# Kernel optimization log

Hardware: AMD Instinct MI355X
Metric: run time of the kernel (lower is better)

The kernel has to match this reference:

```python
import jax, jax.numpy as jnp
import numpy as np

B, L = 16, 2048
D_MODEL, D_INNER, D_STATE, DT_RANK, D_CONV = 128, 256, 16, 8, 4
N_LAYERS, N_CLASSES = 4, 5
EPS = 1e-5


def setup_inputs() -> dict:
    key = jax.random.key(0)
    ks = jax.random.split(key, 12)
    rn = lambda k, shape, s=0.02: jax.random.normal(k, shape, jnp.float32) * s
    A_log = jnp.log(jnp.arange(1, D_STATE + 1, dtype=jnp.float32))  # S4D-real init
    return dict(
        x=jax.random.normal(ks[0], (B, L, 12), jnp.float32),
        enc_w=rn(ks[1], (D_MODEL, 12), 0.1),
        enc_b=jnp.zeros((D_MODEL,), jnp.float32),
        norm_w=jnp.ones((N_LAYERS, D_MODEL), jnp.float32),
        in_proj_w=rn(ks[2], (N_LAYERS, 2 * D_INNER, D_MODEL)),
        conv_w=rn(ks[3], (N_LAYERS, D_INNER, D_CONV), 0.1),
        conv_b=jnp.zeros((N_LAYERS, D_INNER), jnp.float32),
        x_proj_w=rn(ks[4], (N_LAYERS, DT_RANK + 2 * D_STATE, D_INNER)),
        dt_proj_w=rn(ks[5], (N_LAYERS, D_INNER, DT_RANK), 0.1),
        dt_proj_b=rn(ks[6], (N_LAYERS, D_INNER), 0.1),
        A_log=jnp.broadcast_to(A_log, (N_LAYERS, D_INNER, D_STATE)) + 0.0,
        Dp=jnp.ones((N_LAYERS, D_INNER), jnp.float32),
        out_proj_w=rn(ks[7], (N_LAYERS, D_MODEL, D_INNER)),
        norm_f_w=jnp.ones((D_MODEL,), jnp.float32),
        cls_w=rn(ks[8], (N_CLASSES, D_MODEL), 0.05),
        cls_b=jnp.zeros((N_CLASSES,), jnp.float32),
    )


def rmsnorm(x, w):
    return x * jax.lax.rsqrt(jnp.mean(x * x, axis=-1, keepdims=True) + EPS) * w


def causal_depthwise_conv(x, w, b):
    # x: [b, l, di]; w: [di, k]; causal (left) padding, groups=di
    xc = x.transpose(0, 2, 1)  # [b, di, l]
    y = jax.lax.conv_general_dilated(
        xc, w[:, None, :], window_strides=(1,), padding=[(D_CONV - 1, 0)],
        dimension_numbers=("NCH", "OIH", "NCH"), feature_group_count=D_INNER)
    return (y + b[None, :, None]).transpose(0, 2, 1)


def selective_scan(u, delta, A, Bm, Cm, Dv):
    # u, delta: [b,l,di]; A: [di,n]; Bm, Cm: [b,l,n]; Dv: [di]
    dA = jnp.exp(jnp.einsum("bld,dn->bldn", delta, A))          # [b,l,di,n]
    dBu = jnp.einsum("bld,bln,bld->bldn", delta, Bm, u)          # [b,l,di,n]

    def step(h, inp):
        dA_t, dBu_t, C_t = inp
        h = dA_t * h + dBu_t                                     # [b,di,n]
        y = jnp.einsum("bdn,bn->bd", h, C_t)
        return h, y

    h0 = jnp.zeros((u.shape[0], u.shape[2], A.shape[1]), u.dtype)
    xs = (dA.transpose(1, 0, 2, 3), dBu.transpose(1, 0, 2, 3), Cm.transpose(1, 0, 2))
    _, ys = jax.lax.scan(step, h0, xs)
    return ys.transpose(1, 0, 2) + u * Dv


def mamba_block(x, in_w, cw, cb, xp_w, dt_w, dt_b, A_log_i, D_i, out_w):
    xz = jnp.einsum("bld,ed->ble", x, in_w)                      # [b,l,2*di]
    xm, z = xz[..., :D_INNER], xz[..., D_INNER:]
    xm = jax.nn.silu(causal_depthwise_conv(xm, cw, cb))
    x_dbl = jnp.einsum("bld,ed->ble", xm, xp_w)                  # [b,l,dt_rank+2n]
    dt = x_dbl[..., :DT_RANK]
    Bm = x_dbl[..., DT_RANK:DT_RANK + D_STATE]
    Cm = x_dbl[..., DT_RANK + D_STATE:]
    delta = jax.nn.softplus(jnp.einsum("blr,dr->bld", dt, dt_w) + dt_b)
    A = -jnp.exp(A_log_i)
    y = selective_scan(xm, delta, A, Bm, Cm, D_i)
    y = y * jax.nn.silu(z)
    return jnp.einsum("bld,ed->ble", y, out_w)


def reference(x, enc_w, enc_b, norm_w, in_proj_w, conv_w, conv_b, x_proj_w,
              dt_proj_w, dt_proj_b, A_log, Dp, out_proj_w, norm_f_w, cls_w, cls_b):
    h = jnp.einsum("blc,dc->bld", x, enc_w) + enc_b               # conv1d k=1 encoder
    for i in range(N_LAYERS):
        h = mamba_block(rmsnorm(h, norm_w[i]), in_proj_w[i], conv_w[i], conv_b[i],
                        x_proj_w[i], dt_proj_w[i], dt_proj_b[i], A_log[i], Dp[i],
                        out_proj_w[i]) + h
    h = rmsnorm(h, norm_f_w)
    pooled = jnp.mean(h, axis=1)                                  # AdaptiveAvgPool1d(1)
    return pooled @ cls_w.T + cls_b                               # [B, n_classes]
```

## Files before the change

### kernel.cpp

```cpp
#include <hip/hip_runtime.h>
#include <hip/hip_bf16.h>
#include <cstddef>

#define BB 16
#define LL 2048
#define DM 128
#define DI 256
#define DS 16
#define MP (BB*LL)
#define NSEG 64
#define SEGLEN (LL/NSEG)
#define YSTR 264
#define XSTR 40
#define SXS 48

typedef __attribute__((ext_vector_type(8))) short bf16x8;
typedef __attribute__((ext_vector_type(4))) short bf16x4s;
typedef __attribute__((ext_vector_type(8))) unsigned int ux8;
typedef __attribute__((ext_vector_type(4))) float f32x4;
typedef __hip_bfloat16 bf16;
typedef unsigned int uint;

__device__ inline void bf16split(float x, bf16& h, bf16& l) {
  h = __float2bfloat16(x);
  l = __float2bfloat16(x - __bfloat162float(h));
}
__device__ inline float bf2f(bf16 v) { return __bfloat162float(v); }
__device__ inline void split_bits2(float x, short& hs, short& ls) {
  bf16 hb = __float2bfloat16(x);
  bf16 lb = __float2bfloat16(x - __bfloat162float(hb));
  hs = *(short*)&hb;
  ls = *(short*)&lb;
}
__device__ inline short bfbits(float x) {
  bf16 b = __float2bfloat16(x);
  return *(short*)&b;
}
__device__ inline float sigm(float x) {
  return __builtin_amdgcn_rcpf(1.f + __expf(-x));
}
__device__ inline uint pk2(short h, short l) {
  return (uint)(unsigned short)h | ((uint)(unsigned short)l << 16);
}
__device__ inline uint pack_hl(float x) {
  short hs, ls; split_bits2(x, hs, ls);
  return pk2(hs, ls);
}
__device__ inline float unpack_hl(uint w) {
  return __uint_as_float(w << 16) + __uint_as_float(w & 0xffff0000u);
}

__device__ inline float softplus_f(float a) {
  float r = __logf(1.f + __expf(a));
  return a > 15.f ? a : r;
}

__device__ inline void make_powers(float r, float* rp) {
  rp[0] = r;
#pragma unroll
  for (int n = 1; n < 16; n++) {
    int a = (n + 1) >> 1, b = (n + 1) - a;
    rp[n] = rp[a - 1] * rp[b - 1];
  }
}

__device__ inline bool a_is_integer(const float* A_log, int d) {
  bool ok = true;
#pragma unroll
  for (int n = 0; n < DS; n++) {
    float Ad = -__expf(A_log[d * DS + n]);
    ok = ok && (fabsf(Ad + (float)(n + 1)) < 1e-3f);
  }
  return ok;
}

template<bool FAST>
__device__ inline void scan1_lds(int s, int b, int d,
    const float* sx, const short* ubh, const short* ubl,
    const float* __restrict__ dtw, const float* __restrict__ dtb,
    const float* __restrict__ A_log,
    float* __restrict__ sega, float* __restrict__ segh) {
  float wdt[8];
#pragma unroll
  for (int j = 0; j < 8; j++) wdt[j] = dtw[d * 8 + j];
  float bdt = dtb[d];
  float h[DS];
#pragma unroll
  for (int n = 0; n < DS; n++) h[n] = 0.f;
  float R = 1.f;
  float ap[DS];
  if (!FAST) {
#pragma unroll
    for (int n = 0; n < DS; n++) ap[n] = 1.f;
  }
#pragma unroll 4
  for (int t = 0; t < SEGLEN; t++) {
    const float* xr = sx + t * SXS;
    float dt = bdt;
#pragma unroll
    for (int j = 0; j < 8; j++) dt += xr[j] * wdt[j];
    float dl = softplus_f(dt);
    float u = unpack_hl(pk2(ubh[t * 264 + d], ubl[t * 264 + d]));
    float du = dl * u;
    if (FAST) {
      float rp[DS];
      make_powers(__expf(-dl), rp);
      R *= rp[0];
#pragma unroll
      for (int n = 0; n < DS; n++) h[n] = fmaf(rp[n], h[n], du * xr[8 + n]);
    } else {
#pragma unroll
      for (int n = 0; n < DS; n++) {
        float dA = __expf(dl * (-__expf(A_log[d * DS + n])));
        h[n] = fmaf(dA, h[n], du * xr[8 + n]);
        ap[n] *= dA;
      }
    }
  }
  if (FAST) make_powers(R, ap);
  size_t o = ((size_t)s * 4096 + b * 256 + d) * DS;
#pragma unroll
  for (int j = 0; j < 4; j++) {
    *(float4*)(sega + o + 4 * j) = make_float4(ap[4*j], ap[4*j+1], ap[4*j+2], ap[4*j+3]);
    *(float4*)(segh + o + 4 * j) = make_float4(h[4*j], h[4*j+1], h[4*j+2], h[4*j+3]);
  }
}

__global__ __launch_bounds__(256, 2) void gemm_inproj_conv(
    const bf16* __restrict__ Ah, const bf16* __restrict__ Al,
    const bf16* __restrict__ Wh, const bf16* __restrict__ Wl,
    const bf16* __restrict__ Xh, const bf16* __restrict__ Xl,
    const float* __restrict__ cw, const float* __restrict__ cb,
    const float* __restrict__ dtw, const float* __restrict__ dtb,
    const float* __restrict__ A_log,
    uint* __restrict__ zs_pk, uint* __restrict__ u_pk,
    float* __restrict__ C,
    float* __restrict__ sega, float* __restrict__ segh) {
  __shared__ uint  xmb[35 * 260];
  __shared__ short ubh[32 * 264];
  __shared__ short ubl[32 * 264];
  __shared__ float scw[DI * 4 + DI];
  int tid = threadIdx.x;
  {
    float4 w4 = *(const float4*)(cw + tid * 4);
    *(float4*)(scw + tid * 4) = w4;
    scw[DI * 4 + tid] = cb[tid];
  }
  int wave = tid >> 6, lane = tid & 63;
  int r16 = lane & 15, quad = lane >> 4;
  int m0 = blockIdx.x * 32;

  size_t arow[3];
#pragma unroll
  for (int rt = 0; rt < 3; rt++) {
    int rg = m0 - 16 + rt * 16 + r16;
    if (rg < 0) rg = 0;
    arow[rt] = (size_t)rg * DM + quad * 8;
  }
  size_t browx[4], browz[4];
#pragma unroll
  for (int ct = 0; ct < 4; ct++) {
    browx[ct] = (size_t)(wave * 64 + ct * 16 + r16) * DM + quad * 8;
    browz[ct] = (size_t)(256 + wave * 64 + ct * 16 + r16) * DM + quad * 8;
  }
  f32x4 accx[3][4] = {};
  f32x4 accz[2][4] = {};
#pragma unroll
  for (int kk = 0; kk < 4; kk++) {
    int ko = kk * 32;
    bf16x8 ah[3], al[3], bxh[4], bxl[4], bzh[4], bzl[4];
#pragma unroll
    for (int rt = 0; rt < 3; rt++) {
      ah[rt] = *(const bf16x8*)(Ah + arow[rt] + ko);
      al[rt] = *(const bf16x8*)(Al + arow[rt] + ko);
    }
#pragma unroll
    for (int ct = 0; ct < 4; ct++) {
      bxh[ct] = *(const bf16x8*)(Wh + browx[ct] + ko);
      bxl[ct] = *(const bf16x8*)(Wl + browx[ct] + ko);
      bzh[ct] = *(const bf16x8*)(Wh + browz[ct] + ko);
      bzl[ct] = *(const bf16x8*)(Wl + browz[ct] + ko);
    }
#pragma unroll
    for (int rt = 0; rt < 3; rt++)
#pragma unroll
      for (int ct = 0; ct < 4; ct++) {
        accx[rt][ct] = __builtin_amdgcn_mfma_f32_16x16x32_bf16(ah[rt], bxh[ct], accx[rt][ct], 0, 0, 0);
        accx[rt][ct] = __builtin_amdgcn_mfma_f32_16x16x32_bf16(ah[rt], bxl[ct], accx[rt][ct], 0, 0, 0);
        accx[rt][ct] = __builtin_amdgcn_mfma_f32_16x16x32_bf16(al[rt], bxh[ct], accx[rt][ct], 0, 0, 0);
      }
#pragma unroll
    for (int rz = 0; rz < 2; rz++)
#pragma unroll
      for (int ct = 0; ct < 4; ct++) {
        accz[rz][ct] = __builtin_amdgcn_mfma_f32_16x16x32_bf16(ah[rz + 1], bzh[ct], accz[rz][ct], 0, 0, 0);
        accz[rz][ct] = __builtin_amdgcn_mfma_f32_16x16x32_bf16(ah[rz + 1], bzl[ct], accz[rz][ct], 0, 0, 0);
        accz[rz][ct] = __builtin_amdgcn_mfma_f32_16x16x32_bf16(al[rz + 1], bzh[ct], accz[rz][ct], 0, 0, 0);
      }
  }
#pragma unroll
  for (int rz = 0; rz < 2; rz++)
#pragma unroll
    for (int ct = 0; ct < 4; ct++)
#pragma unroll
      for (int r = 0; r < 4; r++) {
        int row = m0 + rz * 16 + quad * 4 + r;
        int col = wave * 64 + ct * 16 + r16;
        float v = accz[rz][ct][r];
        v *= sigm(v);
        zs_pk[(size_t)row * DI + col] = pack_hl(v);
      }
#pragma unroll
  for (int rt = 0; rt < 3; rt++)
#pragma unroll
    for (int ct = 0; ct < 4; ct++)
#pragma unroll
      for (int r = 0; r < 4; r++) {
        int lidx = rt * 16 + quad * 4 + r - 13;
        if (lidx >= 0)
          xmb[lidx * 260 + wave * 64 + ct * 16 + r16] = pack_hl(accx[rt][ct][r]);
      }
  __syncthreads();

  {
    int d = tid;
    float w0 = scw[d * 4], w1 = scw[d * 4 + 1], w2 = scw[d * 4 + 2], w3 = scw[d * 4 + 3];
    float bias = scw[DI * 4 + d];
    float xa = unpack_hl(xmb[0 * 260 + d]);
    float xb = unpack_hl(xmb[1 * 260 + d]);
    float xc = unpack_hl(xmb[2 * 260 + d]);
    int lbase = m0 & (LL - 1);
#pragma unroll 4
    for (int t = 0; t < 32; t++) {
      float xd = unpack_hl(xmb[(t + 3) * 260 + d]);
      int l = lbase + t;
      float x0 = xa * ((l >= 3) ? 1.f : 0.f);
      float x1 = xb * ((l >= 2) ? 1.f : 0.f);
      float x2 = xc * ((l >= 1) ? 1.f : 0.f);
      float c0 = bias + w0 * x0 + w1 * x1 + w2 * x2 + w3 * xd;
      float u = c0 * sigm(c0);
      short hs, ls; split_bits2(u, hs, ls);
      u_pk[(size_t)(m0 + t) * DI + d] = pk2(hs, ls);
      ubh[t * 264 + d] = hs;
      ubl[t * 264 + d] = ls;
      xa = xb; xb = xc; xc = xd;
    }
  }
  __syncthreads();

  float* sx = (float*)xmb;
  {
    int rt0 = (wave == 3) ? 1 : 0;
    int ct0 = (wave == 0) ? 0 : (wave == 1) ? 1 : (wave == 2) ? 2 : 0;
#pragma unroll 1
    for (int tt = 0; tt < 2; tt++) {
      int rt, ct;
      if (tt == 0) { rt = rt0; ct = ct0; }
      else { if (wave >= 2) break; rt = 1; ct = wave + 1; }
      f32x4 a2 = {};
#pragma unroll
      for (int kk = 0; kk < 8; kk++) {
        int k0 = quad * 8 + kk * 32;
        bf16x8 ahh = *(const bf16x8*)(ubh + (rt * 16 + r16) * 264 + k0);
        bf16x8 alo = *(const bf16x8*)(ubl + (rt * 16 + r16) * 264 + k0);
        size_t br = (size_t)(ct * 16 + r16) * DI + quad * 8 + kk * 32;
        bf16x8 bhh = *(const bf16x8*)(Xh + br);
        bf16x8 blo = *(const bf16x8*)(Xl + br);
        a2 = __builtin_amdgcn_mfma_f32_16x16x32_bf16(ahh, bhh, a2, 0, 0, 0);
        a2 = __builtin_amdgcn_mfma_f32_16x16x32_bf16(ahh, blo, a2, 0, 0, 0);
        a2 = __builtin_amdgcn_mfma_f32_16x16x32_bf16(alo, bhh, a2, 0, 0, 0);
      }
#pragma unroll
      for (int r = 0; r < 4; r++) {
        int row = rt * 16 + quad * 4 + r;
        int col = ct * 16 + r16;
        C[(size_t)(m0 + row) * 64 + col] = a2[r];
        sx[row * SXS + col] = a2[r];
      }
    }
  }
  __syncthreads();

  {
    int b = blockIdx.x >> 6, s = blockIdx.x & 63, d = tid;
    if (a_is_integer(A_log, d))
      scan1_lds<true>(s, b, d, sx, ubh, ubl, dtw, dtb, A_log, sega, segh);
    else
      scan1_lds<false>(s, b, d, sx, ubh, ubl, dtw, dtb, A_log, sega, segh);
  }
}

__global__ __launch_bounds__(256) void encoder_kernel(const float* __restrict__ x,
    const float* __restrict__ ew, const float* __restrict__ eb,
    float* __restrict__ h) {
  int idx = blockIdx.x * 256 + threadIdx.x;
  int d = idx & 127, m = idx >> 7;
  float acc = eb[d];
#pragma unroll
  for (int c = 0; c < 12; c++) acc += x[m * 12 + c] * ew[d * 12 + c];
  h[idx] = acc;
}

__global__ void split_w(const float* __restrict__ src, bf16* __restrict__ hi,
                        bf16* __restrict__ lo, int n) {
  int i = blockIdx.x * 256 + threadIdx.x;
  if (i < n) bf16split(src[i], hi[i], lo[i]);
}

__global__ void split_w_pad(const float* __restrict__ src, bf16* __restrict__ hi,
                            bf16* __restrict__ lo) {
  int i = blockIdx.x * 256 + threadIdx.x;
  int l = i >> 14, rem = i & 16383, r = rem >> 8, k = rem & 255;
  float v = (r < 40) ? src[l * 10240 + r * 256 + k] : 0.f;
  bf16split(v, hi[i], lo[i]);
}

__global__ __launch_bounds__(256) void rmsnorm_kernel(const float* __restrict__ x,
    const float* __restrict__ w, bf16* __restrict__ oh, bf16* __restrict__ ol) {
  int lane = threadIdx.x & 63;
  int pos = blockIdx.x * 4 + (threadIdx.x >> 6);
  const float* row = x + (size_t)pos * DM;
  float v0 = row[lane], v1 = row[lane + 64];
  float ss = v0 * v0 + v1 * v1;
#pragma unroll
  for (int off = 1; off < 64; off <<= 1) ss += __shfl_xor(ss, off);
  float sc = rsqrtf(ss * (1.f / DM) + 1e-5f);
  float a = v0 * sc * w[lane], b = v1 * sc * w[lane + 64];
  size_t o = (size_t)pos * DM;
  bf16split(a, oh[o + lane], ol[o + lane]);
  bf16split(b, oh[o + lane + 64], ol[o + lane + 64]);
}

__device__ inline void load_sx(float* sx, const float* xdbl, size_t rbase, int tid) {
#pragma unroll
  for (int j = 0; j < 2; j++) {
    int idx = j * 256 + tid;
    if (idx < 320) {
      int row = idx / 10, c = idx % 10;
      *(float4*)(sx + row * XSTR + c * 4) = *(const float4*)(xdbl + rbase + row * 64 + c * 4);
    }
  }
}

__global__ __launch_bounds__(256) void scan_combine(float* __restrict__ sega,
    const float* __restrict__ segh) {
  int g = blockIdx.x * 256 + threadIdx.x;
  size_t off = (size_t)(g >> 2) * 16 + (g & 3) * 4;
  float4 h0 = make_float4(0.f, 0.f, 0.f, 0.f);
  for (int s = 0; s < NSEG; s++) {
    size_t q = (size_t)s * 65536 + off;
    float4 a = *(float4*)(sega + q);
    float4 hh = *(float4*)(segh + q);
    *(float4*)(sega + q) = h0;
    h0.x = a.x * h0.x + hh.x;
    h0.y = a.y * h0.y + hh.y;
    h0.z = a.z * h0.z + hh.z;
    h0.w = a.w * h0.w + hh.w;
  }
}

template<bool FAST>
__device__ inline void scan2_to_lds(int s, int b, int d, const float* sx,
    const uint* __restrict__ u_pk, const uint* __restrict__ zs_pk,
    const float* __restrict__ dtw, const float* __restrict__ dtb,
    const float* __restrict__ A_log, const float* __restrict__ Dp,
    const float* __restrict__ sega, short* __restrict__ ybuf) {
  float wdt[8];
#pragma unroll
  for (int j = 0; j < 8; j++) wdt[j] = dtw[d * 8 + j];
  float bdt = dtb[d];
  float h[DS];
  size_t o = ((size_t)s * 4096 + b * 256 + d) * DS;
#pragma unroll
  for (int n = 0; n < DS; n++) h[n] = sega[o + n];
  float Dd = Dp[d];
  size_t base = (size_t)b * LL + (size_t)s * SEGLEN;
  const uint* up = u_pk + base * DI + d;
  const uint* zp = zs_pk + base * DI + d;
  uint ub = *up, zb = *zp;
#pragma unroll 4
  for (int t = 0; t < SEGLEN; t++) {
    up += DI; zp += DI;
    uint ub_next = *up;
    uint zb_next = *zp;
    const float* xr = sx + t * XSTR;
    float dt = bdt;
#pragma unroll
    for (int j = 0; j < 8; j++) dt += xr[j] * wdt[j];
    float dl = softplus_f(dt);
    float u = unpack_hl(ub);
    float du = dl * u;
    float acc = 0.f;
    if (FAST) {
      float rp[DS];
      make_powers(__expf(-dl), rp);
#pragma unroll
      for (int n = 0; n < DS; n++) {
        h[n] = fmaf(rp[n], h[n], du * xr[8 + n]);
        acc = fmaf(h[n], xr[24 + n], acc);
      }
    } else {
#pragma unroll
      for (int n = 0; n < DS; n++) {
        float dA = __expf(dl * (-__expf(A_log[d * DS + n])));
        h[n] = fmaf(dA, h[n], du * xr[8 + n]);
        acc = fmaf(h[n], xr[24 + n], acc);
      }
    }
    float zs = unpack_hl(zb);
    float yv = (acc + u * Dd) * zs;
    ybuf[t * YSTR + d] = bfbits(yv);
    ub = ub_next; zb = zb_next;
  }
}

__global__ __launch_bounds__(256, 6) void scan2_outproj(
    const uint* __restrict__ u_pk, const uint* __restrict__ zs_pk,
    const float* __restrict__ xdbl, const float* __restrict__ dtw,
    const float* __restrict__ dtb, const float* __restrict__ A_log,
    const float* __restrict__ Dp, const float* __restrict__ sega,
    const bf16* __restrict__ Wh, const bf16* __restrict__ Wl,
    float* __restrict__ hbuf, const float* __restrict__ nw,
    float* __restrict__ of, bf16* __restrict__ oh, bf16* __restrict__ ol) {
  __shared__ float sx[SEGLEN * XSTR];
  __shared__ short ybuf[32 * YSTR];
  int s = blockIdx.x, b = blockIdx.y;
  int tid = threadIdx.x, d = tid;
  size_t rbase = ((size_t)b * LL + (size_t)s * SEGLEN) * 64;
  load_sx(sx, xdbl, rbase, tid);
  __syncthreads();
  if (a_is_integer(A_log, d))
    scan2_to_lds<true>(s, b, d, sx, u_pk, zs_pk, dtw, dtb, A_log, Dp, sega, ybuf);
  else
    scan2_to_lds<false>(s, b, d, sx, u_pk, zs_pk, dtw, dtb, A_log, Dp, sega, ybuf);
  __syncthreads();
  int wave = tid >> 6, lane = tid & 63;
  int r16 = lane & 15, quad = lane >> 4;
  int n0 = wave * 32;
  size_t brow[2];
#pragma unroll
  for (int j = 0; j < 2; j++)
    brow[j] = (size_t)(n0 + j * 16 + r16) * DI + quad * 8;
  f32x4 acc[2][2] = {};
#pragma unroll
  for (int kk = 0; kk < 8; kk++) {
    int k0 = quad * 8 + kk * 32;
    bf16x8 ah[2], bh[2], bl[2];
#pragma unroll
    for (int i = 0; i < 2; i++)
      ah[i] = *(const bf16x8*)(ybuf + (i * 16 + r16) * YSTR + k0);
#pragma unroll
    for (int j = 0; j < 2; j++) {
      bh[j] = *(const bf16x8*)(Wh + brow[j] + kk * 32);
      bl[j] = *(const bf16x8*)(Wl + brow[j] + kk * 32);
    }
#pragma unroll
    for (int i = 0; i < 2; i++)
#pragma unroll
      for (int j = 0; j < 2; j++) {
        acc[i][j] = __builtin_amdgcn_mfma_f32_16x16x32_bf16(ah[i], bh[j], acc[i][j], 0, 0, 0);
        acc[i][j] = __builtin_amdgcn_mfma_f32_16x16x32_bf16(ah[i], bl[j], acc[i][j], 0, 0, 0);
      }
  }
  __syncthreads();
  float* tile = (float*)ybuf;
#pragma unroll
  for (int i = 0; i < 2; i++)
#pragma unroll
    for (int j = 0; j < 2; j++)
#pragma unroll
      for (int r = 0; r < 4; r++) {
        int rl = i * 16 + quad * 4 + r;
        int col = n0 + j * 16 + r16;
        tile[rl * 132 + col] = acc[i][j][r];
      }
  __syncthreads();
  size_t mbase = (size_t)b * LL + (size_t)s * SEGLEN;
#pragma unroll
  for (int it = 0; it < 4; it++) {
    int idx = it * 256 + tid;
    int row = idx >> 5, c4 = idx & 31;
    size_t g = (mbase + row) * DM + c4 * 4;
    float4 hv = *(float4*)(hbuf + g);
    const float* tp = tile + row * 132 + c4 * 4;
    float4 v = make_float4(tp[0] + hv.x, tp[1] + hv.y, tp[2] + hv.z, tp[3] + hv.w);
    *(float4*)(hbuf + g) = v;
    float ss = v.x * v.x + v.y * v.y + v.z * v.z + v.w * v.w;
    ss += __shfl_xor(ss, 1);
    ss += __shfl_xor(ss, 2);
    ss += __shfl_xor(ss, 4);
    ss += __shfl_xor(ss, 8);
    ss += __shfl_xor(ss, 16);
    float sc = rsqrtf(ss * (1.f / DM) + 1e-5f);
    float4 w4 = *(const float4*)(nw + c4 * 4);
    float n0v = v.x * sc * w4.x, n1v = v.y * sc * w4.y;
    float n2v = v.z * sc * w4.z, n3v = v.w * sc * w4.w;
    if (of) *(float4*)(of + g) = make_float4(n0v, n1v, n2v, n3v);
    short h0s, l0s, h1s, l1s, h2s, l2s, h3s, l3s;
    split_bits2(n0v, h0s, l0s); split_bits2(n1v, h1s, l1s);
    split_bits2(n2v, h2s, l2s); split_bits2(n3v, h3s, l3s);
    bf16x4s hb, lb;
    hb[0] = h0s; hb[1] = h1s; hb[2] = h2s; hb[3] = h3s;
    lb[0] = l0s; lb[1] = l1s; lb[2] = l2s; lb[3] = l3s;
    *(bf16x4s*)(oh + g) = hb;
    *(bf16x4s*)(ol + g) = lb;
  }
}

__global__ __launch_bounds__(256) void pool_partial(const float* __restrict__ fn,
    float* __restrict__ partial) {
  __shared__ float red[256];
  int b = blockIdx.x, c = blockIdx.y;
  int tid = threadIdx.x;
  int d = tid & 127, rp_ = tid >> 7;
  float s = 0.f;
  size_t base = (size_t)b * LL + c * 256;
  for (int i = 0; i < 128; i++) {
    int row = i * 2 + rp_;
    s += fn[(base + row) * DM + d];
  }
  red[tid] = s;
  __syncthreads();
  if (tid < 128) partial[((size_t)b * 8 + c) * 128 + tid] = red[tid] + red[tid + 128];
}

__global__ void pool_reduce(const float* __restrict__ partial,
    float* __restrict__ pooled) {
  int idx = blockIdx.x * 256 + threadIdx.x;
  int b = idx >> 7, d = idx & 127;
  float s = 0.f;
#pragma unroll
  for (int c = 0; c < 8; c++) s += partial[((size_t)b * 8 + c) * 128 + d];
  pooled[idx] = s * (1.f / LL);
}

__global__ void cls_kernel(const float* __restrict__ pooled,
    const float* __restrict__ cw, const float* __restrict__ cb,
    float* __restrict__ out) {
  int t = threadIdx.x;
  if (t < 80) {
    int b = t / 5, c = t % 5;
    float acc = cb[c];
    for (int d = 0; d < DM; d++) acc += pooled[b * DM + d] * cw[c * DM + d];
    out[t] = acc;
  }
}

extern "C" void kernel_launch(void* const* d_in, const int* in_sizes, int n_in,
                              void* d_out, int out_size, void* d_ws, size_t ws_size,
                              hipStream_t stream) {
  const float* x         = (const float*)d_in[0];
  const float* enc_w     = (const float*)d_in[1];
  const float* enc_b     = (const float*)d_in[2];
  const float* norm_w    = (const float*)d_in[3];
  const float* in_proj_w = (const float*)d_in[4];
  const float* conv_w    = (const float*)d_in[5];
  const float* conv_b    = (const float*)d_in[6];
  const float* x_proj_w  = (const float*)d_in[7];
  const float* dt_proj_w = (const float*)d_in[8];
  const float* dt_proj_b = (const float*)d_in[9];
  const float* A_log     = (const float*)d_in[10];
  const float* Dp        = (const float*)d_in[11];
  const float* out_proj_w= (const float*)d_in[12];
  const float* norm_f_w  = (const float*)d_in[13];
  const float* cls_w     = (const float*)d_in[14];
  const float* cls_b     = (const float*)d_in[15];
  float* out = (float*)d_out;

  float* ws = (float*)d_ws;
  float* h       = ws;
  float* xdbl    = ws + 4194304;
  float* sega    = ws + 6291456;
  float* segh    = ws + 10485760;
  uint*  zs_pk   = (uint*)(ws + 14680064);
  uint*  u_pk    = (uint*)(ws + 23068672);
  uint*  xm_pk   = (uint*)(ws + 31457280);
  float* partial = ws + 39845888;
  float* pooled  = ws + 39862272;
  bf16* u0     = (bf16*)(ws + 39864320);
  bf16* xn_hi  = u0;
  bf16* xn_lo  = u0 + 4194304;
  bf16* wip_hi = u0 + 8388608;
  bf16* wip_lo = wip_hi + 262144;
  bf16* wxp_hi = wip_lo + 262144;
  bf16* wxp_lo = wxp_hi + 65536;
  bf16* wop_hi = wxp_lo + 65536;
  bf16* wop_lo = wop_hi + 131072;
  float* fnorm = (float*)xm_pk;

  split_w<<<1024, 256, 0, stream>>>(in_proj_w, wip_hi, wip_lo, 262144);
  split_w_pad<<<256, 256, 0, stream>>>(x_proj_w, wxp_hi, wxp_lo);
  split_w<<<512, 256, 0, stream>>>(out_proj_w, wop_hi, wop_lo, 131072);

  encoder_kernel<<<MP * DM / 256, 256, 0, stream>>>(x, enc_w, enc_b, h);
  rmsnorm_kernel<<<MP / 4, 256, 0, stream>>>(h, norm_w, xn_hi, xn_lo);

  for (int i = 0; i < 4; i++) {
    gemm_inproj_conv<<<MP / 32, 256, 0, stream>>>(xn_hi, xn_lo,
        wip_hi + i * 65536, wip_lo + i * 65536,
        wxp_hi + i * 16384, wxp_lo + i * 16384,
        conv_w + i * DI * 4, conv_b + i * DI,
        dt_proj_w + i * 2048, dt_proj_b + i * DI, A_log + i * DI * DS,
        zs_pk, u_pk, xdbl, sega, segh);
    scan_combine<<<64, 256, 0, stream>>>(sega, segh);
    scan2_outproj<<<dim3(NSEG, BB), 256, 0, stream>>>(u_pk, zs_pk, xdbl,
        dt_proj_w + i * 2048, dt_proj_b + i * DI, A_log + i * DI * DS,
        Dp + i * DI, sega, wop_hi + i * 32768, wop_lo + i * 32768, h,
        (i < 3) ? norm_w + (i + 1) * DM : norm_f_w,
        (i < 3) ? nullptr : fnorm, xn_hi, xn_lo);
  }

  pool_partial<<<dim3(BB, 8), 256, 0, stream>>>(fnorm, partial);
  pool_reduce<<<8, 256, 0, stream>>>(partial, pooled);
  cls_kernel<<<1, 128, 0, stream>>>(pooled, cls_w, cls_b, out);
}
```

Baseline: 661.8 us.

## Move z-branch in_proj GEMM into scan kernel and keep gate in LDS

The z half of the in_proj GEMM and its SiLU gate move out of the in_proj/conv kernel and into the scan/out_proj kernel. The gate is computed per 16-row half directly into shared memory, so the packed zs buffer no longer has to be written to and read back from global memory each layer. The cost is more shared memory and registers in the scan kernel, which drops its occupancy hint from 6 to 4 blocks. Extra barriers and the z GEMM itself now sit serially between the two scan halves.

```diff
diff --git a/kernel.cpp b/kernel.cpp
--- a/kernel.cpp
+++ b/kernel.cpp
@@ -133,7 +133,7 @@
     const float* __restrict__ cw, const float* __restrict__ cb,
     const float* __restrict__ dtw, const float* __restrict__ dtb,
     const float* __restrict__ A_log,
-    uint* __restrict__ zs_pk, uint* __restrict__ u_pk,
+    uint* __restrict__ u_pk,
     float* __restrict__ C,
     float* __restrict__ sega, float* __restrict__ segh) {
   __shared__ uint  xmb[35 * 260];
@@ -157,18 +157,15 @@
     if (rg < 0) rg = 0;
     arow[rt] = (size_t)rg * DM + quad * 8;
   }
-  size_t browx[4], browz[4];
-#pragma unroll
-  for (int ct = 0; ct < 4; ct++) {
+  size_t browx[4];
+#pragma unroll
+  for (int ct = 0; ct < 4; ct++)
     browx[ct] = (size_t)(wave * 64 + ct * 16 + r16) * DM + quad * 8;
-    browz[ct] = (size_t)(256 + wave * 64 + ct * 16 + r16) * DM + quad * 8;
-  }
   f32x4 accx[3][4] = {};
-  f32x4 accz[2][4] = {};
 #pragma unroll
   for (int kk = 0; kk < 4; kk++) {
     int ko = kk * 32;
-    bf16x8 ah[3], al[3], bxh[4], bxl[4], bzh[4], bzl[4];
+    bf16x8 ah[3], al[3], bxh[4], bxl[4];
 #pragma unroll
     for (int rt = 0; rt < 3; rt++) {
       ah[rt] = *(const bf16x8*)(Ah + arow[rt] + ko);
@@ -178,8 +175,6 @@
     for (int ct = 0; ct < 4; ct++) {
       bxh[ct] = *(const bf16x8*)(Wh + browx[ct] + ko);
       bxl[ct] = *(const bf16x8*)(Wl + browx[ct] + ko);
-      bzh[ct] = *(const bf16x8*)(Wh + browz[ct] + ko);
-      bzl[ct] = *(const bf16x8*)(Wl + browz[ct] + ko);
     }
 #pragma unroll
     for (int rt = 0; rt < 3; rt++)
@@ -189,27 +184,7 @@
         accx[rt][ct] = __builtin_amdgcn_mfma_f32_16x16x32_bf16(ah[rt], bxl[ct], accx[rt][ct], 0, 0, 0);
         accx[rt][ct] = __builtin_amdgcn_mfma_f32_16x16x32_bf16(al[rt], bxh[ct], accx[rt][ct], 0, 0, 0);
       }
-#pragma unroll
-    for (int rz = 0; rz < 2; rz++)
-#pragma unroll
-      for (int ct = 0; ct < 4; ct++) {
-        accz[rz][ct] = __builtin_amdgcn_mfma_f32_16x16x32_bf16(ah[rz + 1], bzh[ct], accz[rz][ct], 0, 0, 0);
-        accz[rz][ct] = __builtin_amdgcn_mfma_f32_16x16x32_bf16(ah[rz + 1], bzl[ct], accz[rz][ct], 0, 0, 0);
-        accz[rz][ct] = __builtin_amdgcn_mfma_f32_16x16x32_bf16(al[rz + 1], bzh[ct], accz[rz][ct], 0, 0, 0);
-      }
-  }
-#pragma unroll
-  for (int rz = 0; rz < 2; rz++)
-#pragma unroll
-    for (int ct = 0; ct < 4; ct++)
-#pragma unroll
-      for (int r = 0; r < 4; r++) {
-        int row = m0 + rz * 16 + quad * 4 + r;
-        int col = wave * 64 + ct * 16 + r16;
-        float v = accz[rz][ct][r];
-        v *= sigm(v);
-        zs_pk[(size_t)row * DI + col] = pack_hl(v);
-      }
+  }
 #pragma unroll
   for (int rt = 0; rt < 3; rt++)
 #pragma unroll
@@ -359,30 +334,52 @@
   }
 }
 
+__device__ inline void zgemm_half(int hh, size_t mbase, int wave, int r16, int quad,
+    const bf16* xnh, const bf16* xnl,
+    const bf16* __restrict__ Wih, const bf16* __restrict__ Wil,
+    uint* zbuf) {
+  size_t ar = (mbase + hh * 16 + r16) * DM + quad * 8;
+  size_t br[4];
+#pragma unroll
+  for (int ct = 0; ct < 4; ct++)
+    br[ct] = (size_t)(256 + wave * 64 + ct * 16 + r16) * DM + quad * 8;
+  f32x4 acc[4] = {};
+#pragma unroll
+  for (int kk = 0; kk < 4; kk++) {
+    int ko = kk * 32;
+    bf16x8 ah = *(const bf16x8*)(xnh + ar + ko);
+    bf16x8 al = *(const bf16x8*)(xnl + ar + ko);
+    bf16x8 bh[4], bl[4];
+#pragma unroll
+    for (int ct = 0; ct < 4; ct++) {
+      bh[ct] = *(const bf16x8*)(Wih + br[ct] + ko);
+      bl[ct] = *(const bf16x8*)(Wil + br[ct] + ko);
+    }
+#pragma unroll
+    for (int ct = 0; ct < 4; ct++) {
+      acc[ct] = __builtin_amdgcn_mfma_f32_16x16x32_bf16(ah, bh[ct], acc[ct], 0, 0, 0);
+      acc[ct] = __builtin_amdgcn_mfma_f32_16x16x32_bf16(ah, bl[ct], acc[ct], 0, 0, 0);
+      acc[ct] = __builtin_amdgcn_mfma_f32_16x16x32_bf16(al, bh[ct], acc[ct], 0, 0, 0);
+    }
+  }
+#pragma unroll
+  for (int ct = 0; ct < 4; ct++)
+#pragma unroll
+    for (int r = 0; r < 4; r++) {
+      float v = acc[ct][r];
+      v *= sigm(v);
+      zbuf[(quad * 4 + r) * 260 + wave * 64 + ct * 16 + r16] = pack_hl(v);
+    }
+}
+
 template<bool FAST>
-__device__ inline void scan2_to_lds(int s, int b, int d, const float* sx,
-    const uint* __restrict__ u_pk, const uint* __restrict__ zs_pk,
-    const float* __restrict__ dtw, const float* __restrict__ dtb,
-    const float* __restrict__ A_log, const float* __restrict__ Dp,
-    const float* __restrict__ sega, short* __restrict__ ybuf) {
-  float wdt[8];
-#pragma unroll
-  for (int j = 0; j < 8; j++) wdt[j] = dtw[d * 8 + j];
-  float bdt = dtb[d];
-  float h[DS];
-  size_t o = ((size_t)s * 4096 + b * 256 + d) * DS;
-#pragma unroll
-  for (int n = 0; n < DS; n++) h[n] = sega[o + n];
-  float Dd = Dp[d];
-  size_t base = (size_t)b * LL + (size_t)s * SEGLEN;
-  const uint* up = u_pk + base * DI + d;
-  const uint* zp = zs_pk + base * DI + d;
-  uint ub = *up, zb = *zp;
+__device__ inline void scan2_half(int t0, int d, const float* sx, const uint* zbuf,
+    const uint*& up, uint& ub, const float* wdt, float bdt,
+    const float* __restrict__ A_log, float Dd, float* h, short* ybuf) {
 #pragma unroll 4
-  for (int t = 0; t < SEGLEN; t++) {
-    up += DI; zp += DI;
+  for (int t = t0; t < t0 + 16; t++) {
+    up += DI;
     uint ub_next = *up;
-    uint zb_next = *zp;
     const float* xr = sx + t * XSTR;
     float dt = bdt;
 #pragma unroll
@@ -407,35 +404,62 @@
         acc = fmaf(h[n], xr[24 + n], acc);
       }
     }
-    float zs = unpack_hl(zb);
+    float zs = unpack_hl(zbuf[(t & 15) * 260 + d]);
     float yv = (acc + u * Dd) * zs;
     ybuf[t * YSTR + d] = bfbits(yv);
-    ub = ub_next; zb = zb_next;
-  }
-}
-
-__global__ __launch_bounds__(256, 6) void scan2_outproj(
-    const uint* __restrict__ u_pk, const uint* __restrict__ zs_pk,
+    ub = ub_next;
+  }
+}
+
+__global__ __launch_bounds__(256, 4) void scan2_outproj(
+    const uint* __restrict__ u_pk,
+    const bf16* __restrict__ Wih, const bf16* __restrict__ Wil,
     const float* __restrict__ xdbl, const float* __restrict__ dtw,
     const float* __restrict__ dtb, const float* __restrict__ A_log,
     const float* __restrict__ Dp, const float* __restrict__ sega,
     const bf16* __restrict__ Wh, const bf16* __restrict__ Wl,
     float* __restrict__ hbuf, const float* __restrict__ nw,
-    float* __restrict__ of, bf16* __restrict__ oh, bf16* __restrict__ ol) {
+    float* __restrict__ of, bf16* oh, bf16* ol) {
   __shared__ float sx[SEGLEN * XSTR];
   __shared__ short ybuf[32 * YSTR];
+  __shared__ uint zbuf[16 * 260];
   int s = blockIdx.x, b = blockIdx.y;
   int tid = threadIdx.x, d = tid;
   size_t rbase = ((size_t)b * LL + (size_t)s * SEGLEN) * 64;
   load_sx(sx, xdbl, rbase, tid);
-  __syncthreads();
-  if (a_is_integer(A_log, d))
-    scan2_to_lds<true>(s, b, d, sx, u_pk, zs_pk, dtw, dtb, A_log, Dp, sega, ybuf);
-  else
-    scan2_to_lds<false>(s, b, d, sx, u_pk, zs_pk, dtw, dtb, A_log, Dp, sega, ybuf);
-  __syncthreads();
   int wave = tid >> 6, lane = tid & 63;
   int r16 = lane & 15, quad = lane >> 4;
+  size_t mbase = (size_t)b * LL + (size_t)s * SEGLEN;
+
+  float wdt[8];
+#pragma unroll
+  for (int j = 0; j < 8; j++) wdt[j] = dtw[d * 8 + j];
+  float bdt = dtb[d];
+  float hst[DS];
+  {
+    size_t o = ((size_t)s * 4096 + b * 256 + d) * DS;
+#pragma unroll
+    for (int n = 0; n < DS; n++) hst[n] = sega[o + n];
+  }
+  float Dd = Dp[d];
+  const uint* up = u_pk + mbase * DI + d;
+  uint ub = *up;
+  bool fast = a_is_integer(A_log, d);
+
+  const bf16* xnh = (const bf16*)oh;
+  const bf16* xnl = (const bf16*)ol;
+
+  zgemm_half(0, mbase, wave, r16, quad, xnh, xnl, Wih, Wil, zbuf);
+  __syncthreads();
+  if (fast) scan2_half<true>(0, d, sx, zbuf, up, ub, wdt, bdt, A_log, Dd, hst, ybuf);
+  else      scan2_half<false>(0, d, sx, zbuf, up, ub, wdt, bdt, A_log, Dd, hst, ybuf);
+  __syncthreads();
+  zgemm_half(1, mbase, wave, r16, quad, xnh, xnl, Wih, Wil, zbuf);
+  __syncthreads();
+  if (fast) scan2_half<true>(16, d, sx, zbuf, up, ub, wdt, bdt, A_log, Dd, hst, ybuf);
+  else      scan2_half<false>(16, d, sx, zbuf, up, ub, wdt, bdt, A_log, Dd, hst, ybuf);
+  __syncthreads();
+
   int n0 = wave * 32;
   size_t brow[2];
 #pragma unroll
@@ -475,7 +499,6 @@
         tile[rl * 132 + col] = acc[i][j][r];
       }
   __syncthreads();
-  size_t mbase = (size_t)b * LL + (size_t)s * SEGLEN;
 #pragma unroll
   for (int it = 0; it < 4; it++) {
     int idx = it * 256 + tid;
@@ -587,6 +610,7 @@
   bf16* wop_hi = wxp_lo + 65536;
   bf16* wop_lo = wop_hi + 131072;
   float* fnorm = (float*)xm_pk;
+  (void)zs_pk;
 
   split_w<<<1024, 256, 0, stream>>>(in_proj_w, wip_hi, wip_lo, 262144);
   split_w_pad<<<256, 256, 0, stream>>>(x_proj_w, wxp_hi, wxp_lo);
@@ -601,10 +625,11 @@
         wxp_hi + i * 16384, wxp_lo + i * 16384,
         conv_w + i * DI * 4, conv_b + i * DI,
         dt_proj_w + i * 2048, dt_proj_b + i * DI, A_log + i * DI * DS,
-        zs_pk, u_pk, xdbl, sega, segh);
+        u_pk, xdbl, sega, segh);
     scan_combine<<<64, 256, 0, stream>>>(sega, segh);
-    scan2_outproj<<<dim3(NSEG, BB), 256, 0, stream>>>(u_pk, zs_pk, xdbl,
-        dt_proj_w + i * 2048, dt_proj_b + i * DI, A_log + i * DI * DS,
+    scan2_outproj<<<dim3(NSEG, BB), 256, 0, stream>>>(u_pk,
+        wip_hi + i * 65536, wip_lo + i * 65536,
+        xdbl, dt_proj_w + i * 2048, dt_proj_b + i * DI, A_log + i * DI * DS,
         Dp + i * DI, sega, wop_hi + i * 32768, wop_lo + i * 32768, h,
         (i < 3) ? norm_w + (i + 1) * DM : norm_f_w,
         (i < 3) ? nullptr : fnorm, xn_hi, xn_lo);
```

Measured after the change: 694.5 us. 4.9% more time.
